# Kernel optimization log

Hardware: AMD Instinct MI355X
Metric: run time of the kernel (lower is better)

Reference implementation:

```python
import jax, jax.numpy as jnp
import numpy as np

N_NODES = 100000
N_EDGES = 1600000
N_FEAT = 128
HIDDEN = 16
EMBED = 128
N_GRAPHS = 64


def setup_inputs() -> dict:
    key = jax.random.key(0)
    ks = jax.random.split(key, 6)
    x = jax.random.normal(ks[0], (N_NODES, N_FEAT), dtype=jnp.float32)
    edge_index = jax.random.randint(ks[1], (2, N_EDGES), 0, N_NODES, dtype=jnp.int32)
    batch = jnp.sort(jax.random.randint(ks[2], (N_NODES,), 0, N_GRAPHS, dtype=jnp.int32))
    W1 = jax.random.normal(ks[3], (N_FEAT, HIDDEN), dtype=jnp.float32) * (1.0 / np.sqrt(N_FEAT))
    b1 = jnp.zeros((HIDDEN,), dtype=jnp.float32)
    W2 = jax.random.normal(ks[4], (HIDDEN, EMBED), dtype=jnp.float32) * (1.0 / np.sqrt(HIDDEN))
    b2 = jnp.zeros((EMBED,), dtype=jnp.float32)
    return {"x": x, "edge_index": edge_index, "batch": batch,
            "W1": W1, "b1": b1, "W2": W2, "b2": b2}


def _gcn_conv(x, W, b, src, dst, dinv):
    # x' = D^{-1/2} (A + I) D^{-1/2} (x W) + b ; (src, dst) already include self-loops
    h = x @ W                                   # [N, out]
    norm = dinv[src] * dinv[dst]                # [E']
    msg = h[src] * norm[:, None]                # gather + scale
    out = jax.ops.segment_sum(msg, dst, num_segments=x.shape[0])  # scatter-add
    return out + b


def reference(x, edge_index, batch, W1, b1, W2, b2):
    n = x.shape[0]
    loop = jnp.arange(n, dtype=edge_index.dtype)
    src = jnp.concatenate([edge_index[0], loop])  # add self-loops
    dst = jnp.concatenate([edge_index[1], loop])
    deg = jax.ops.segment_sum(jnp.ones_like(dst, dtype=x.dtype), dst, num_segments=n)
    dinv = jnp.where(deg > 0, jax.lax.rsqrt(deg), 0.0)

    h = _gcn_conv(x, W1, b1, src, dst, dinv)
    h = jax.nn.relu(h)
    # dropout(p=0.2) is identity in eval mode
    h = _gcn_conv(h, W2, b2, src, dst, dinv)

    # mean pooling over graphs in the batch
    sums = jax.ops.segment_sum(h, batch, num_segments=N_GRAPHS)          # [G, EMBED]
    cnt = jax.ops.segment_sum(jnp.ones((n,), dtype=h.dtype), batch, num_segments=N_GRAPHS)
    return sums / jnp.maximum(cnt, 1.0)[:, None]
```

## Files before the change

kernel.cpp:

```cpp
#include <hip/hip_runtime.h>

#define HIDDEN 16
#define N_FEAT 128
#define EMBED 128
#define N_GRAPHS 64
#define BSH 8
#define MAXB 512

typedef unsigned int uint;

__device__ inline uint pk2(float a, float b) {
    uint ua = __float_as_uint(a), ub = __float_as_uint(b);
    ua = (ua + 0x7FFFu + ((ua >> 16) & 1u)) >> 16;
    ub = (ub + 0x7FFFu + ((ub >> 16) & 1u)) & 0xFFFF0000u;
    return ua | ub;
}
__device__ inline float2 upk2(uint w) {
    return make_float2(__uint_as_float(w << 16), __uint_as_float(w & 0xFFFF0000u));
}

__global__ void __launch_bounds__(1024)
k_hist(const int* __restrict__ dst, int n_edges, int nbuck, int* __restrict__ ghist) {
    __shared__ int h[MAXB];
    for (int i = threadIdx.x; i < MAXB; i += 1024) h[i] = 0;
    __syncthreads();
    int base = blockIdx.x * 4096;
#pragma unroll
    for (int j = 0; j < 4; j++) {
        int e = base + j * 1024 + threadIdx.x;
        if (e < n_edges) atomicAdd(&h[dst[e] >> BSH], 1);
    }
    __syncthreads();
    for (int b = threadIdx.x; b < nbuck; b += 1024)
        if (h[b]) atomicAdd(&ghist[b], h[b]);
}

__global__ void k_scan(const int* __restrict__ ghist, int nbuck,
                       int* __restrict__ gbase, int* __restrict__ gfill) {
    __shared__ int s[MAXB];
    int t = threadIdx.x;
    s[t] = (t < nbuck) ? ghist[t] : 0;
    __syncthreads();
    for (int st = 1; st < MAXB; st <<= 1) {
        int v = (t >= st) ? s[t - st] : 0;
        __syncthreads();
        s[t] += v;
        __syncthreads();
    }
    if (t < nbuck) {
        int excl = s[t] - ghist[t];
        gbase[t] = excl;
        gfill[t] = excl;
    }
}

__global__ void __launch_bounds__(1024)
k_part(const int* __restrict__ src, const int* __restrict__ dst,
       int n_edges, int nbuck, int* __restrict__ gfill, uint* __restrict__ ebuf) {
    __shared__ int hcnt[MAXB];
    __shared__ int hexcl[MAXB];
    __shared__ int hrank[MAXB];
    __shared__ int hbase[MAXB];
    __shared__ uint stage[4096];
    int tid = threadIdx.x;
    for (int i = tid; i < MAXB; i += 1024) { hcnt[i] = 0; hrank[i] = 0; }
    __syncthreads();
    int base = blockIdx.x * 4096;
    int cnt = min(4096, n_edges - base);
    int s_[4], d_[4];
#pragma unroll
    for (int j = 0; j < 4; j++) {
        int k = j * 1024 + tid;
        if (k < cnt) {
            s_[j] = src[base + k]; d_[j] = dst[base + k];
            atomicAdd(&hcnt[d_[j] >> BSH], 1);
        }
    }
    __syncthreads();
    if (tid < MAXB) hexcl[tid] = hcnt[tid];
    __syncthreads();
    for (int st = 1; st < MAXB; st <<= 1) {
        int v = 0;
        if (tid < MAXB && tid >= st) v = hexcl[tid - st];
        __syncthreads();
        if (tid < MAXB) hexcl[tid] += v;
        __syncthreads();
    }
    if (tid < nbuck && hcnt[tid] > 0)
        hbase[tid] = atomicAdd(&gfill[tid], hcnt[tid]);
    __syncthreads();
#pragma unroll
    for (int j = 0; j < 4; j++) {
        int k = j * 1024 + tid;
        if (k < cnt) {
            int b = d_[j] >> BSH;
            int r = atomicAdd(&hrank[b], 1);
            stage[hexcl[b] - hcnt[b] + r] = ((uint)s_[j] << 8) | ((uint)d_[j] & 255u);
        }
    }
    __syncthreads();
    for (int t = tid; t < cnt; t += 1024) {
        uint e = stage[t];
        int lo = 0, hi = MAXB - 1;
        while (lo < hi) {
            int mid = (lo + hi) >> 1;
            if (t < hexcl[mid]) hi = mid; else lo = mid + 1;
        }
        int b = lo;
        ebuf[hbase[b] + (t - (hexcl[b] - hcnt[b]))] = e;
    }
}

__global__ void __launch_bounds__(1024)
k_csr(const uint* __restrict__ ebuf, const int* __restrict__ gbase,
      const int* __restrict__ ghist, int n,
      int* __restrict__ deg, int* __restrict__ rowp, int* __restrict__ col) {
    __shared__ int nh[256], nexcl[256], nrank[256];
    int b = blockIdx.x;
    int tid = threadIdx.x;
    int seg0 = gbase[b];
    int cnt = ghist[b];
    int nb0 = b << BSH;
    if (tid < 256) { nh[tid] = 0; nrank[tid] = 0; }
    __syncthreads();
    for (int t = tid; t < cnt; t += 1024)
        atomicAdd(&nh[ebuf[seg0 + t] & 255u], 1);
    __syncthreads();
    if (tid < 256) nexcl[tid] = nh[tid];
    __syncthreads();
    for (int st = 1; st < 256; st <<= 1) {
        int v = 0;
        if (tid < 256 && tid >= st) v = nexcl[tid - st];
        __syncthreads();
        if (tid < 256) nexcl[tid] += v;
        __syncthreads();
    }
    if (tid < 256) {
        int node = nb0 + tid;
        if (node < n) {
            deg[node]  = nh[tid];
            rowp[node] = seg0 + nexcl[tid] - nh[tid];
        }
    }
    __syncthreads();
    for (int t = tid; t < cnt; t += 1024) {
        uint e = ebuf[seg0 + t];
        int ln = (int)(e & 255u);
        int r = atomicAdd(&nrank[ln], 1);
        col[seg0 + (nexcl[ln] - nh[ln]) + r] = (int)(e >> 8);
    }
}

__global__ void k_gemm1(const float* __restrict__ x, const float* __restrict__ W1,
                        const int* __restrict__ deg, float* __restrict__ dinv,
                        uint* __restrict__ Hs2, int n) {
    __shared__ float Ws[N_FEAT * HIDDEN];
    int tid = threadIdx.x;
    {
        const float4* w4 = (const float4*)W1;
        float4* s4 = (float4*)Ws;
        s4[tid * 2]     = w4[tid * 2];
        s4[tid * 2 + 1] = w4[tid * 2 + 1];
    }
    __syncthreads();
    int i = blockIdx.x * blockDim.x + tid;
    if (i >= n) return;

    float acc[HIDDEN];
#pragma unroll
    for (int o = 0; o < HIDDEN; o++) acc[o] = 0.f;

    const float4* xr = (const float4*)(x + (size_t)i * N_FEAT);
#pragma unroll 8
    for (int k4 = 0; k4 < N_FEAT / 4; k4++) {
        float4 xv = xr[k4];
        const float* w0 = &Ws[(k4 * 4 + 0) * HIDDEN];
        const float* w1 = &Ws[(k4 * 4 + 1) * HIDDEN];
        const float* w2 = &Ws[(k4 * 4 + 2) * HIDDEN];
        const float* w3 = &Ws[(k4 * 4 + 3) * HIDDEN];
#pragma unroll
        for (int o = 0; o < HIDDEN; o++)
            acc[o] += xv.x * w0[o] + xv.y * w1[o] + xv.z * w2[o] + xv.w * w3[o];
    }
    float di = rsqrtf((float)deg[i] + 1.0f);
    dinv[i] = di;
    uint o8[8];
#pragma unroll
    for (int j = 0; j < 8; j++) o8[j] = pk2(acc[2 * j] * di, acc[2 * j + 1] * di);
    uint4* hp = (uint4*)(Hs2 + (size_t)i * 8);
    hp[0] = make_uint4(o8[0], o8[1], o8[2], o8[3]);
    hp[1] = make_uint4(o8[4], o8[5], o8[6], o8[7]);
}

template <int LAYER>
__global__ void k_pull(const uint* __restrict__ V2, const int* __restrict__ rowptr,
                       const int* __restrict__ deg, const int* __restrict__ col,
                       const float* __restrict__ dinv, const float* __restrict__ b1,
                       uint* __restrict__ Q2, float2* __restrict__ R2, int n) {
    int wid = (blockIdx.x * blockDim.x + threadIdx.x) >> 6;
    int lane = threadIdx.x & 63;
    if (wid >= n) return;
    int f  = lane & 7;
    int es = lane >> 3;
    int start = rowptr[wid];
    int dg = deg[wid];
    float ax = 0.f, ay = 0.f;
    for (int j = es; j < dg; j += 8) {
        int s = col[start + j];
        float2 v = upk2(V2[(size_t)s * 8 + f]);
        ax += v.x; ay += v.y;
    }
    ax += __shfl_xor(ax, 8, 64);  ay += __shfl_xor(ay, 8, 64);
    ax += __shfl_xor(ax, 16, 64); ay += __shfl_xor(ay, 16, 64);
    ax += __shfl_xor(ax, 32, 64); ay += __shfl_xor(ay, 32, 64);
    if (lane < 8) {
        float2 h = upk2(V2[(size_t)wid * 8 + f]);
        float tx = ax + h.x, ty = ay + h.y;
        float di = dinv[wid];
        if (LAYER == 1) {
            float qa = fmaxf(di * tx + b1[2 * f],     0.f) * di;
            float qb = fmaxf(di * ty + b1[2 * f + 1], 0.f) * di;
            Q2[(size_t)wid * 8 + f] = pk2(qa, qb);
        } else {
            R2[(size_t)wid * 8 + f] = make_float2(di * tx, di * ty);
        }
    }
}

__global__ void k_pool(const float* __restrict__ R, const int* __restrict__ batch,
                       float* __restrict__ S, float* __restrict__ cnt, int n) {
    __shared__ float ls[8 * HIDDEN];
    __shared__ float lc[8];
    int tid = threadIdx.x;
    if (tid < 8) lc[tid] = 0.f;
    if (tid < 8 * HIDDEN) ls[tid] = 0.f;
    __syncthreads();

    int i0 = blockIdx.x * 256;
    int g0 = batch[i0 < n ? i0 : (n - 1)];
    int i = i0 + tid;
    if (i < n) {
        int g = batch[i];
        const float* r = R + (size_t)i * HIDDEN;
        int off = g - g0;
        if (off >= 0 && off < 8) {
#pragma unroll
            for (int o = 0; o < HIDDEN; o++) atomicAdd(&ls[off * HIDDEN + o], r[o]);
            atomicAdd(&lc[off], 1.f);
        } else {
#pragma unroll
            for (int o = 0; o < HIDDEN; o++) atomicAdd(&S[(size_t)g * HIDDEN + o], r[o]);
            atomicAdd(&cnt[g], 1.f);
        }
    }
    __syncthreads();
    if (tid < 8 * HIDDEN) {
        int b = tid >> 4, o = tid & 15;
        int g = g0 + b;
        float v = ls[b * HIDDEN + o];
        if (v != 0.f && g < N_GRAPHS) atomicAdd(&S[(size_t)g * HIDDEN + o], v);
    }
    if (tid < 8) {
        int g = g0 + tid;
        float c = lc[tid];
        if (c != 0.f && g < N_GRAPHS) atomicAdd(&cnt[g], c);
    }
}

__global__ void k_out(const float* __restrict__ S, const float* __restrict__ cnt,
                      const float* __restrict__ W2, const float* __restrict__ b2,
                      float* __restrict__ out) {
    int g = blockIdx.x;
    int e = threadIdx.x;
    float c = cnt[g];
    float acc = 0.f;
#pragma unroll
    for (int k = 0; k < HIDDEN; k++) acc += S[g * HIDDEN + k] * W2[k * EMBED + e];
    out[g * EMBED + e] = (c > 0.f) ? (acc / c + b2[e]) : 0.f;
}

extern "C" void kernel_launch(void* const* d_in, const int* in_sizes, int n_in,
                              void* d_out, int out_size, void* d_ws, size_t ws_size,
                              hipStream_t stream) {
    const float* x     = (const float*)d_in[0];
    const int*   ei    = (const int*)  d_in[1];
    const int*   batch = (const int*)  d_in[2];
    const float* W1    = (const float*)d_in[3];
    const float* b1    = (const float*)d_in[4];
    const float* W2    = (const float*)d_in[5];
    const float* b2    = (const float*)d_in[6];
    float* out = (float*)d_out;

    const int n       = in_sizes[2];
    const int n_edges = in_sizes[1] / 2;
    const int* srcp = ei;
    const int* dstp = ei + n_edges;
    const int nbuck = (n + 255) >> BSH;

    uint*  Hs2   = (uint*)d_ws;
    uint*  Q2    = Hs2 + (size_t)n * 8;
    float* dinv  = (float*)(Q2 + (size_t)n * 8);
    int*   deg   = (int*)(dinv + n);
    int*   rowp  = deg + n;
    int*   col   = rowp + n;
    uint*  ebuf  = (uint*)(col + n_edges);
    int*   ghist = (int*)(ebuf + n_edges);
    int*   gbase = ghist + MAXB;
    int*   gfill = gbase + MAXB;
    float* S     = (float*)(gfill + MAXB);
    float* cnt   = S + N_GRAPHS * HIDDEN;
    float* R     = (float*)ebuf;

    hipMemsetAsync(ghist, 0, MAXB * sizeof(int), stream);
    hipMemsetAsync(S, 0, (N_GRAPHS * HIDDEN + N_GRAPHS) * sizeof(float), stream);

    const int pb4k = (n_edges + 4095) / 4096;
    k_hist <<<pb4k, 1024, 0, stream>>>(dstp, n_edges, nbuck, ghist);
    k_scan <<<1, MAXB, 0, stream>>>(ghist, nbuck, gbase, gfill);
    k_part <<<pb4k, 1024, 0, stream>>>(srcp, dstp, n_edges, nbuck, gfill, ebuf);
    k_csr  <<<nbuck, 1024, 0, stream>>>(ebuf, gbase, ghist, n, deg, rowp, col);

    const int nb = (n + 255) / 256;
    k_gemm1<<<nb, 256, 0, stream>>>(x, W1, deg, dinv, Hs2, n);

    const int pullb = (n * 64 + 255) / 256;
    k_pull<1><<<pullb, 256, 0, stream>>>(Hs2, rowp, deg, col, dinv, b1, Q2, (float2*)R, n);
    k_pull<2><<<pullb, 256, 0, stream>>>(Q2,  rowp, deg, col, dinv, b1, Hs2, (float2*)R, n);

    k_pool <<<nb, 256, 0, stream>>>(R, batch, S, cnt, n);
    k_out  <<<N_GRAPHS, EMBED, 0, stream>>>(S, cnt, W2, b2, out);
}
```

Before: 255.1 us.

## Double edges per partition block, store bucket ids, pack layer-2 output as bf16, merge memsets

The partition and histogram kernels now process 8192 edges per block instead of 4096. The partition kernel also stores each staged edge's bucket id in shared memory, which replaces the per-element binary search during scatter. The second pull kernel writes its output as packed bf16 instead of float2, and the pool kernel unpacks it, halving that intermediate's traffic at the cost of extra rounding. The two memsets are merged into one by reordering the workspace layout.

```diff
diff --git a/kernel.cpp b/kernel.cpp
--- a/kernel.cpp
+++ b/kernel.cpp
@@ -6,6 +6,7 @@
 #define N_GRAPHS 64
 #define BSH 8
 #define MAXB 512
+#define EPT 8
 
 typedef unsigned int uint;
 
@@ -24,9 +25,9 @@
     __shared__ int h[MAXB];
     for (int i = threadIdx.x; i < MAXB; i += 1024) h[i] = 0;
     __syncthreads();
-    int base = blockIdx.x * 4096;
-#pragma unroll
-    for (int j = 0; j < 4; j++) {
+    int base = blockIdx.x * (EPT * 1024);
+#pragma unroll
+    for (int j = 0; j < EPT; j++) {
         int e = base + j * 1024 + threadIdx.x;
         if (e < n_edges) atomicAdd(&h[dst[e] >> BSH], 1);
     }
@@ -58,18 +59,19 @@
 k_part(const int* __restrict__ src, const int* __restrict__ dst,
        int n_edges, int nbuck, int* __restrict__ gfill, uint* __restrict__ ebuf) {
     __shared__ int hcnt[MAXB];
-    __shared__ int hexcl[MAXB];
+    __shared__ int hincl[MAXB];
     __shared__ int hrank[MAXB];
     __shared__ int hbase[MAXB];
-    __shared__ uint stage[4096];
+    __shared__ uint stage[EPT * 1024];
+    __shared__ unsigned short sbuck[EPT * 1024];
     int tid = threadIdx.x;
     for (int i = tid; i < MAXB; i += 1024) { hcnt[i] = 0; hrank[i] = 0; }
     __syncthreads();
-    int base = blockIdx.x * 4096;
-    int cnt = min(4096, n_edges - base);
-    int s_[4], d_[4];
-#pragma unroll
-    for (int j = 0; j < 4; j++) {
+    int base = blockIdx.x * (EPT * 1024);
+    int cnt = min(EPT * 1024, n_edges - base);
+    int s_[EPT], d_[EPT];
+#pragma unroll
+    for (int j = 0; j < EPT; j++) {
         int k = j * 1024 + tid;
         if (k < cnt) {
             s_[j] = src[base + k]; d_[j] = dst[base + k];
@@ -77,37 +79,33 @@
         }
     }
     __syncthreads();
-    if (tid < MAXB) hexcl[tid] = hcnt[tid];
+    if (tid < MAXB) hincl[tid] = hcnt[tid];
     __syncthreads();
     for (int st = 1; st < MAXB; st <<= 1) {
         int v = 0;
-        if (tid < MAXB && tid >= st) v = hexcl[tid - st];
-        __syncthreads();
-        if (tid < MAXB) hexcl[tid] += v;
+        if (tid < MAXB && tid >= st) v = hincl[tid - st];
+        __syncthreads();
+        if (tid < MAXB) hincl[tid] += v;
         __syncthreads();
     }
     if (tid < nbuck && hcnt[tid] > 0)
         hbase[tid] = atomicAdd(&gfill[tid], hcnt[tid]);
     __syncthreads();
 #pragma unroll
-    for (int j = 0; j < 4; j++) {
+    for (int j = 0; j < EPT; j++) {
         int k = j * 1024 + tid;
         if (k < cnt) {
             int b = d_[j] >> BSH;
             int r = atomicAdd(&hrank[b], 1);
-            stage[hexcl[b] - hcnt[b] + r] = ((uint)s_[j] << 8) | ((uint)d_[j] & 255u);
+            int pos = hincl[b] - hcnt[b] + r;
+            stage[pos] = ((uint)s_[j] << 8) | ((uint)d_[j] & 255u);
+            sbuck[pos] = (unsigned short)b;
         }
     }
     __syncthreads();
     for (int t = tid; t < cnt; t += 1024) {
-        uint e = stage[t];
-        int lo = 0, hi = MAXB - 1;
-        while (lo < hi) {
-            int mid = (lo + hi) >> 1;
-            if (t < hexcl[mid]) hi = mid; else lo = mid + 1;
-        }
-        int b = lo;
-        ebuf[hbase[b] + (t - (hexcl[b] - hcnt[b]))] = e;
+        int b = sbuck[t];
+        ebuf[hbase[b] + (t - (hincl[b] - hcnt[b]))] = stage[t];
     }
 }
 
@@ -115,7 +113,7 @@
 k_csr(const uint* __restrict__ ebuf, const int* __restrict__ gbase,
       const int* __restrict__ ghist, int n,
       int* __restrict__ deg, int* __restrict__ rowp, int* __restrict__ col) {
-    __shared__ int nh[256], nexcl[256], nrank[256];
+    __shared__ int nh[256], nincl[256], nrank[256];
     int b = blockIdx.x;
     int tid = threadIdx.x;
     int seg0 = gbase[b];
@@ -126,20 +124,20 @@
     for (int t = tid; t < cnt; t += 1024)
         atomicAdd(&nh[ebuf[seg0 + t] & 255u], 1);
     __syncthreads();
-    if (tid < 256) nexcl[tid] = nh[tid];
+    if (tid < 256) nincl[tid] = nh[tid];
     __syncthreads();
     for (int st = 1; st < 256; st <<= 1) {
         int v = 0;
-        if (tid < 256 && tid >= st) v = nexcl[tid - st];
-        __syncthreads();
-        if (tid < 256) nexcl[tid] += v;
+        if (tid < 256 && tid >= st) v = nincl[tid - st];
+        __syncthreads();
+        if (tid < 256) nincl[tid] += v;
         __syncthreads();
     }
     if (tid < 256) {
         int node = nb0 + tid;
         if (node < n) {
             deg[node]  = nh[tid];
-            rowp[node] = seg0 + nexcl[tid] - nh[tid];
+            rowp[node] = seg0 + nincl[tid] - nh[tid];
         }
     }
     __syncthreads();
@@ -147,7 +145,7 @@
         uint e = ebuf[seg0 + t];
         int ln = (int)(e & 255u);
         int r = atomicAdd(&nrank[ln], 1);
-        col[seg0 + (nexcl[ln] - nh[ln]) + r] = (int)(e >> 8);
+        col[seg0 + (nincl[ln] - nh[ln]) + r] = (int)(e >> 8);
     }
 }
 
@@ -196,7 +194,7 @@
 __global__ void k_pull(const uint* __restrict__ V2, const int* __restrict__ rowptr,
                        const int* __restrict__ deg, const int* __restrict__ col,
                        const float* __restrict__ dinv, const float* __restrict__ b1,
-                       uint* __restrict__ Q2, float2* __restrict__ R2, int n) {
+                       uint* __restrict__ out2, int n) {
     int wid = (blockIdx.x * blockDim.x + threadIdx.x) >> 6;
     int lane = threadIdx.x & 63;
     if (wid >= n) return;
@@ -220,14 +218,14 @@
         if (LAYER == 1) {
             float qa = fmaxf(di * tx + b1[2 * f],     0.f) * di;
             float qb = fmaxf(di * ty + b1[2 * f + 1], 0.f) * di;
-            Q2[(size_t)wid * 8 + f] = pk2(qa, qb);
+            out2[(size_t)wid * 8 + f] = pk2(qa, qb);
         } else {
-            R2[(size_t)wid * 8 + f] = make_float2(di * tx, di * ty);
-        }
-    }
-}
-
-__global__ void k_pool(const float* __restrict__ R, const int* __restrict__ batch,
+            out2[(size_t)wid * 8 + f] = pk2(di * tx, di * ty);
+        }
+    }
+}
+
+__global__ void k_pool(const uint* __restrict__ R2, const int* __restrict__ batch,
                        float* __restrict__ S, float* __restrict__ cnt, int n) {
     __shared__ float ls[8 * HIDDEN];
     __shared__ float lc[8];
@@ -241,7 +239,12 @@
     int i = i0 + tid;
     if (i < n) {
         int g = batch[i];
-        const float* r = R + (size_t)i * HIDDEN;
+        float r[HIDDEN];
+#pragma unroll
+        for (int j = 0; j < 8; j++) {
+            float2 v = upk2(R2[(size_t)i * 8 + j]);
+            r[2 * j] = v.x; r[2 * j + 1] = v.y;
+        }
         int off = g - g0;
         if (off >= 0 && off < 8) {
 #pragma unroll
@@ -305,28 +308,27 @@
     int*   col   = rowp + n;
     uint*  ebuf  = (uint*)(col + n_edges);
     int*   ghist = (int*)(ebuf + n_edges);
-    int*   gbase = ghist + MAXB;
+    float* S     = (float*)(ghist + MAXB);
+    float* cnt   = S + N_GRAPHS * HIDDEN;
+    int*   gbase = (int*)(cnt + N_GRAPHS);
     int*   gfill = gbase + MAXB;
-    float* S     = (float*)(gfill + MAXB);
-    float* cnt   = S + N_GRAPHS * HIDDEN;
-    float* R     = (float*)ebuf;
-
-    hipMemsetAsync(ghist, 0, MAXB * sizeof(int), stream);
-    hipMemsetAsync(S, 0, (N_GRAPHS * HIDDEN + N_GRAPHS) * sizeof(float), stream);
-
-    const int pb4k = (n_edges + 4095) / 4096;
-    k_hist <<<pb4k, 1024, 0, stream>>>(dstp, n_edges, nbuck, ghist);
+    uint*  R2    = ebuf;
+
+    hipMemsetAsync(ghist, 0, (MAXB + N_GRAPHS * HIDDEN + N_GRAPHS) * sizeof(int), stream);
+
+    const int pb8k = (n_edges + EPT * 1024 - 1) / (EPT * 1024);
+    k_hist <<<pb8k, 1024, 0, stream>>>(dstp, n_edges, nbuck, ghist);
     k_scan <<<1, MAXB, 0, stream>>>(ghist, nbuck, gbase, gfill);
-    k_part <<<pb4k, 1024, 0, stream>>>(srcp, dstp, n_edges, nbuck, gfill, ebuf);
+    k_part <<<pb8k, 1024, 0, stream>>>(srcp, dstp, n_edges, nbuck, gfill, ebuf);
     k_csr  <<<nbuck, 1024, 0, stream>>>(ebuf, gbase, ghist, n, deg, rowp, col);
 
     const int nb = (n + 255) / 256;
     k_gemm1<<<nb, 256, 0, stream>>>(x, W1, deg, dinv, Hs2, n);
 
     const int pullb = (n * 64 + 255) / 256;
-    k_pull<1><<<pullb, 256, 0, stream>>>(Hs2, rowp, deg, col, dinv, b1, Q2, (float2*)R, n);
-    k_pull<2><<<pullb, 256, 0, stream>>>(Q2,  rowp, deg, col, dinv, b1, Hs2, (float2*)R, n);
-
-    k_pool <<<nb, 256, 0, stream>>>(R, batch, S, cnt, n);
+    k_pull<1><<<pullb, 256, 0, stream>>>(Hs2, rowp, deg, col, dinv, b1, Q2, n);
+    k_pull<2><<<pullb, 256, 0, stream>>>(Q2,  rowp, deg, col, dinv, b1, R2, n);
+
+    k_pool <<<nb, 256, 0, stream>>>(R2, batch, S, cnt, n);
     k_out  <<<N_GRAPHS, EMBED, 0, stream>>>(S, cnt, W2, b2, out);
 }
```

After: 242.4 us. -5.0%, faster.
